# Optimization experiments

Hardware: AMD Instinct MI355X
Metric: run time of the kernel (lower is better)

The kernel has to match this reference:

```python
import jax, jax.numpy as jnp
import numpy as np

N = 20000
E = 640000
D = 128
NORM_FACTOR = 100.0
LN_EPS = 1e-5


def _layer_norm(x, g, b):
    mu = jnp.mean(x, axis=-1, keepdims=True)
    var = jnp.var(x, axis=-1, keepdims=True)
    return (x - mu) * jax.lax.rsqrt(var + LN_EPS) * g + b


def setup_inputs() -> dict:
    key = jax.random.key(0)
    ks = jax.random.split(key, 16)

    def lin(k, fan_in, shape):
        bound = 1.0 / np.sqrt(fan_in)
        return jax.random.uniform(k, shape, jnp.float32, -bound, bound)

    h = jax.random.normal(ks[0], (N, D), jnp.float32)
    distances = jax.random.uniform(ks[1], (E, 1), jnp.float32)
    edges = jax.random.randint(ks[2], (2, E), 0, N, jnp.int64)
    node_mask = jnp.ones((N, 1), jnp.float32)
    edge_mask = jnp.ones((E, 1), jnp.float32)

    return {
        "h": h, "distances": distances, "node_mask": node_mask, "edge_mask": edge_mask,
        # linear: in->out
        "lin_w": lin(ks[3], D, (D, D)), "lin_b": lin(ks[4], D, (D,)),
        # att_mlp: (2D+1)->2D -> 2D->D -> D->1
        "att_w1": lin(ks[5], 2 * D + 1, (2 * D, 2 * D + 1)), "att_b1": lin(ks[5], 2 * D + 1, (2 * D,)),
        "att_w2": lin(ks[6], 2 * D, (D, 2 * D)), "att_b2": lin(ks[6], 2 * D, (D,)),
        "att_w3": lin(ks[7], D, (1, D)), "att_b3": lin(ks[7], D, (1,)),
        # node_mlp: D->D, LN, SiLU, D->D
        "nm_w1": lin(ks[8], D, (D, D)), "nm_b1": lin(ks[8], D, (D,)),
        "nm_ln_g": jnp.ones((D,), jnp.float32), "nm_ln_b": jnp.zeros((D,), jnp.float32),
        "nm_w2": lin(ks[9], D, (D, D)), "nm_b2": lin(ks[9], D, (D,)),
        # final LayerNorm
        "ln_g": jnp.ones((D,), jnp.float32), "ln_b": jnp.zeros((D,), jnp.float32),
        "edges": edges,
    }


def reference(h, distances, node_mask, edge_mask,
              lin_w, lin_b, att_w1, att_b1, att_w2, att_b2, att_w3, att_b3,
              nm_w1, nm_b1, nm_ln_g, nm_ln_b, nm_w2, nm_b2, ln_g, ln_b, edges):
    x = h @ lin_w.T + lin_b                                  # [N, D]
    row, col = edges[0], edges[1]
    x_row = x[row]                                           # [E, D]
    x_col = x[col]                                           # [E, D]

    # DenseAtt
    d = distances * edge_mask
    x_cat = jnp.concatenate([x_row, x_col, d], axis=1)       # [E, 2D+1]
    a = jax.nn.silu(x_cat @ att_w1.T + att_b1)
    a = jax.nn.silu(a @ att_w2.T + att_b2)
    att = jax.nn.sigmoid(a @ att_w3.T + att_b3) * edge_mask  # [E, 1]

    agg = x_col * att                                        # [E, D]
    out = jax.ops.segment_sum(agg, row, num_segments=N) / NORM_FACTOR

    # node_mlp + residual
    o = out @ nm_w1.T + nm_b1
    o = jax.nn.silu(_layer_norm(o, nm_ln_g, nm_ln_b))
    o = o @ nm_w2.T + nm_b2
    hh = o + x

    hh = _layer_norm(hh, ln_g, ln_b)
    hh = jax.nn.silu(hh)                                     # act = SiLU
    return hh
```

## Files before the change

kernel.cpp:

```cpp
#include <hip/hip_runtime.h>
#include <hip/hip_bf16.h>

#define N_NODES 20000
#define E_EDGES 640000
#define DIM 128
#define CAP 96
#define EPB 64
#define NPB 8
#define XST 264

typedef __attribute__((ext_vector_type(8))) short bf16x8;
typedef __attribute__((ext_vector_type(4))) float f32x4;
typedef __attribute__((ext_vector_type(4))) unsigned u32x4;

#define LOG2E 1.44269504f
__device__ __forceinline__ float fsilu(float x) {
    return x * __builtin_amdgcn_rcpf(1.f + __builtin_amdgcn_exp2f(-LOG2E * x));
}
__device__ __forceinline__ float fsig(float x) {
    return __builtin_amdgcn_rcpf(1.f + __builtin_amdgcn_exp2f(-LOG2E * x));
}

__device__ __forceinline__ unsigned short f2bf(float x) {
    union { float f; unsigned u; } v; v.f = x;
    unsigned r = (v.u + 0x7fffu + ((v.u >> 16) & 1u)) >> 16;
    return (unsigned short)r;
}
__device__ __forceinline__ float bf2f(unsigned short s) {
    union { unsigned u; float f; } v; v.u = ((unsigned)s) << 16;
    return v.f;
}
__device__ __forceinline__ unsigned pack_bf16(float lo, float hi) {
    union { float f; unsigned u; } a, b; a.f = lo; b.f = hi;
    unsigned ul = a.u + 0x8000u, uh = b.u + 0x8000u;
    return __builtin_amdgcn_perm(uh, ul, 0x07060302u);
}

#define PRE_PREP_BLOCKS 64
#define PRE_LIN_BLOCKS  625
#define PRE_ADJ_BLOCKS  2500
__global__ __launch_bounds__(256) void pre_kernel(
    const float* __restrict__ w1, const float* __restrict__ w2,
    unsigned short* __restrict__ w1b, float* __restrict__ w1p,
    unsigned short* __restrict__ w2b,
    const float* __restrict__ h, const float* __restrict__ lw,
    const float* __restrict__ lb, float* __restrict__ x,
    unsigned short* __restrict__ xb,
    const int* __restrict__ edges,
    const float* __restrict__ dist, const float* __restrict__ emask,
    int* __restrict__ cnt,
    int* __restrict__ adjc, float2* __restrict__ dm, int E) {
    __shared__ float hs[32][128];
    int b = blockIdx.x;
    int t = threadIdx.x;

    if (b < PRE_PREP_BLOCKS) {
        int i = b * 256 + t;
        const int stride = PRE_PREP_BLOCKS * 256;
        for (int idx = i; idx < 256 * 256; idx += stride) {
            int o = idx >> 8, k = idx & 255;
            w1b[idx] = f2bf(w1[o * 257 + k]);
        }
        for (int idx = i; idx < 128 * 256; idx += stride) {
            int n2 = idx >> 8, p = idx & 255;
            int bb = p & ~31, off = p & 31;
            int ksrc = bb + (off >> 1) + ((off & 1) << 4);
            w2b[idx] = f2bf(w2[n2 * 256 + ksrc]);
        }
        for (int idx = i; idx < 256; idx += stride) {
            int bb = idx & ~31, off = idx & 31;
            int ksrc = bb + (off >> 1) + ((off & 1) << 4);
            w1p[idx] = w1[ksrc * 257 + 256];
        }
    } else if (b < PRE_PREP_BLOCKS + PRE_LIN_BLOCKS) {
        int nb = b - PRE_PREP_BLOCKS;
        int n0 = nb * 32;
        int ch = t & 127, g = t >> 7;
#pragma unroll
        for (int j = 0; j < 16; ++j) hs[g * 16 + j][ch] = h[(size_t)(n0 + g * 16 + j) * DIM + ch];
        __syncthreads();
        float acc[16];
#pragma unroll
        for (int j = 0; j < 16; ++j) acc[j] = 0.f;
        for (int kc = 0; kc < 128; kc += 4) {
            float4 wv = *(const float4*)&lw[(size_t)ch * DIM + kc];
#pragma unroll
            for (int j = 0; j < 16; ++j) {
                float4 hv = *(const float4*)&hs[g * 16 + j][kc];
                acc[j] += wv.x * hv.x + wv.y * hv.y + wv.z * hv.z + wv.w * hv.w;
            }
        }
        float bias = lb[ch];
#pragma unroll
        for (int j = 0; j < 16; ++j) {
            float v = acc[j] + bias;
            int n = n0 + g * 16 + j;
            x[(size_t)n * DIM + ch] = v;
            xb[(size_t)n * DIM + ch] = f2bf(v);
        }
    } else {
        int e = (b - PRE_PREP_BLOCKS - PRE_LIN_BLOCKS) * 256 + t;
        if (e < E) {
            int r = edges[e];
            int col = edges[E + e];
            float em = emask[e];
            float dv = dist[e] * em;
            int slot = atomicAdd(&cnt[r], 1);
            if (slot < CAP) {
                adjc[(size_t)r * CAP + slot] = col;
                float2 de; de.x = dv; de.y = em;
                dm[(size_t)r * CAP + slot] = de;
            }
        }
    }
}

__global__ __launch_bounds__(1024) void scan_kernel(const int* __restrict__ cnt,
                                                    int* __restrict__ off) {
    __shared__ int wsum[16], wbase[16];
    int t = threadIdx.x;
    int lane = t & 63, wid = t >> 6;
    int base = t * 20;
    int loc[20];
    int s = 0;
#pragma unroll
    for (int i = 0; i < 20; ++i) {
        int idx = base + i;
        int v = 0;
        if (idx < N_NODES) { v = cnt[idx]; v = v > CAP ? CAP : v; }
        loc[i] = s; s += v;
    }
    int inc = s;
#pragma unroll
    for (int d = 1; d < 64; d <<= 1) {
        int u = __shfl_up(inc, d);
        if (lane >= d) inc += u;
    }
    if (lane == 63) wsum[wid] = inc;
    __syncthreads();
    if (t < 16) {
        int v = wsum[t];
        int inc2 = v;
#pragma unroll
        for (int d = 1; d < 16; d <<= 1) {
            int u = __shfl_up(inc2, d);
            if (t >= d) inc2 += u;
        }
        wbase[t] = inc2 - v;
        if (t == 15) off[N_NODES] = inc2;
    }
    __syncthreads();
    int ex = wbase[wid] + inc - s;
#pragma unroll
    for (int i = 0; i < 20; ++i) {
        int idx = base + i;
        if (idx < N_NODES) off[idx] = ex + loc[i];
    }
}

#define MID_PRC_BLOCKS 1250
#define MID_FLAT_BLOCKS 2500
__global__ __launch_bounds__(256) void mid_kernel(
    const unsigned short* __restrict__ xb,
    const unsigned short* __restrict__ w1b,
    const float* __restrict__ b1,
    unsigned short* __restrict__ prb, unsigned short* __restrict__ pcb,
    const int* __restrict__ adjc, const float2* __restrict__ dm,
    const int* __restrict__ cnt, const int* __restrict__ off,
    int4* __restrict__ flat) {
    int b = blockIdx.x;
    if (b < MID_PRC_BLOCKS) {
        int n0 = b * 16;
        int w = threadIdx.x >> 6, lane = threadIdx.x & 63;
        int lrow = lane & 15, quad = lane >> 4;

        bf16x8 a[4];
#pragma unroll
        for (int kk = 0; kk < 4; ++kk)
            a[kk] = *(const bf16x8*)&xb[(size_t)(n0 + lrow) * DIM + kk * 32 + quad * 8];

        f32x4 z = {0.f, 0.f, 0.f, 0.f};
#pragma unroll
        for (int i = 0; i < 8; ++i) {
            int gt = w * 8 + i;
            int half = gt >> 4;
            int obase = (gt & 15) * 16;
            f32x4 acc = z;
#pragma unroll
            for (int kk = 0; kk < 4; ++kk) {
                bf16x8 bfrag = *(const bf16x8*)&w1b[(size_t)(obase + lrow) * 256 + half * 128 + kk * 32 + quad * 8];
                acc = __builtin_amdgcn_mfma_f32_16x16x32_bf16(a[kk], bfrag, acc, 0, 0, 0);
            }
            int o = obase + lrow;
            if (half == 0) {
                float bias = b1[o];
#pragma unroll
                for (int r = 0; r < 4; ++r)
                    prb[(size_t)(n0 + quad * 4 + r) * 256 + o] = f2bf(acc[r] + bias);
            } else {
#pragma unroll
                for (int r = 0; r < 4; ++r)
                    pcb[(size_t)(n0 + quad * 4 + r) * 256 + o] = f2bf(acc[r]);
            }
        }
    } else {
        int fb = b - MID_PRC_BLOCKS;
        int n0 = fb * NPB;
        int jg = threadIdx.x >> 5, l = threadIdx.x & 31;
        int n = n0 + jg;
        int c = cnt[n]; c = c > CAP ? CAP : c;
        int o = off[n];
        const int* al = adjc + (size_t)n * CAP;
        const float2* dl = dm + (size_t)n * CAP;
        for (int i = l; i < c; i += 32) {
            float2 de = dl[i];
            int4 wv;
            union { float f; int i; } u1, u2; u1.f = de.x; u2.f = de.y;
            wv.x = n; wv.y = al[i]; wv.z = u1.i; wv.w = u2.i;
            flat[o + i] = wv;
        }
    }
}

__global__ __launch_bounds__(512, 4) void edge_kernel(
    const unsigned short* __restrict__ prb, const unsigned short* __restrict__ pcb,
    const int4* __restrict__ flat, const int* __restrict__ off,
    const float* __restrict__ w1p,
    const unsigned short* __restrict__ w2b, const float* __restrict__ b2,
    const float* __restrict__ w3, const float* __restrict__ b3v,
    float* __restrict__ attv) {
    __shared__ unsigned short buf[EPB * XST];
    __shared__ float part[8][EPB];
    __shared__ float w1ps[256];

    int tid = threadIdx.x;
    int eb = blockIdx.x * EPB;
    int count = off[N_NODES];

    if (tid < 256) w1ps[tid] = w1p[tid];

    int ge = tid >> 3, cb = tid & 7;
    int eidx = eb + ge;
    int4 fv;
    if (eidx < count) fv = flat[eidx];
    else { fv.x = 0; fv.y = 0; fv.z = 0; fv.w = 0; }
    const unsigned short* prow = prb + (size_t)fv.x * 256 + cb * 32;
    const unsigned short* pcp  = pcb + (size_t)fv.y * 256 + cb * 32;
    union { int i; float f; } ud; ud.i = fv.z;
    float d = ud.f;

    bf16x8 pA0 = *(const bf16x8*)&prow[0];
    bf16x8 pB0 = *(const bf16x8*)&prow[16];
    bf16x8 qA0 = *(const bf16x8*)&pcp[0];
    bf16x8 qB0 = *(const bf16x8*)&pcp[16];
    bf16x8 pA1 = *(const bf16x8*)&prow[8];
    bf16x8 pB1 = *(const bf16x8*)&prow[24];
    bf16x8 qA1 = *(const bf16x8*)&pcp[8];
    bf16x8 qB1 = *(const bf16x8*)&pcp[24];

    int wave = tid >> 6, lane = tid & 63;
    int lrow = lane & 15, quad = lane >> 4;
    int n2 = wave * 16 + lrow;
    float bias2 = b2[n2];
    float w3v = w3[n2];

    __syncthreads();

    {
        const float* wp = &w1ps[cb * 32];
        unsigned u[16];
#pragma unroll
        for (int l = 0; l < 8; ++l) {
            float s0 = bf2f((unsigned short)pA0[l]) + bf2f((unsigned short)qA0[l]) + d * wp[2 * l];
            float s1 = bf2f((unsigned short)pB0[l]) + bf2f((unsigned short)qB0[l]) + d * wp[2 * l + 1];
            u[l] = pack_bf16(fsilu(s0), fsilu(s1));
        }
#pragma unroll
        for (int l = 0; l < 8; ++l) {
            float s0 = bf2f((unsigned short)pA1[l]) + bf2f((unsigned short)qA1[l]) + d * wp[16 + 2 * l];
            float s1 = bf2f((unsigned short)pB1[l]) + bf2f((unsigned short)qB1[l]) + d * wp[16 + 2 * l + 1];
            u[8 + l] = pack_bf16(fsilu(s0), fsilu(s1));
        }
        u32x4* w4 = (u32x4*)&buf[ge * XST + cb * 32];
        u32x4 v0 = {u[0], u[1], u[2], u[3]};
        u32x4 v1 = {u[4], u[5], u[6], u[7]};
        u32x4 v2 = {u[8], u[9], u[10], u[11]};
        u32x4 v3 = {u[12], u[13], u[14], u[15]};
        w4[0] = v0; w4[1] = v1; w4[2] = v2; w4[3] = v3;
    }
    __syncthreads();

    f32x4 zz = {0.f, 0.f, 0.f, 0.f};
    f32x4 acc2[4];
#pragma unroll
    for (int mt = 0; mt < 4; ++mt) acc2[mt] = zz;

    for (int kk = 0; kk < 8; ++kk) {
        int ka = kk * 32 + quad * 8;
        bf16x8 bfrag = *(const bf16x8*)&w2b[(size_t)n2 * 256 + ka];
#pragma unroll
        for (int mt = 0; mt < 4; ++mt) {
            bf16x8 a = *(bf16x8*)&buf[(mt * 16 + lrow) * XST + ka];
            acc2[mt] = __builtin_amdgcn_mfma_f32_16x16x32_bf16(a, bfrag, acc2[mt], 0, 0, 0);
        }
    }

    float s[4][4];
#pragma unroll
    for (int mt = 0; mt < 4; ++mt)
#pragma unroll
        for (int r = 0; r < 4; ++r)
            s[mt][r] = fsilu(acc2[mt][r] + bias2) * w3v;
#pragma unroll
    for (int off2 = 1; off2 < 16; off2 <<= 1) {
#pragma unroll
        for (int mt = 0; mt < 4; ++mt)
#pragma unroll
            for (int r = 0; r < 4; ++r)
                s[mt][r] += __shfl_xor(s[mt][r], off2);
    }
    if (lrow == 0) {
#pragma unroll
        for (int mt = 0; mt < 4; ++mt)
#pragma unroll
            for (int r = 0; r < 4; ++r)
                part[wave][mt * 16 + quad * 4 + r] = s[mt][r];
    }
    __syncthreads();

    if (tid < EPB) {
        int idx = eb + tid;
        if (idx < count) {
            float ssum = b3v[0];
#pragma unroll
            for (int w = 0; w < 8; ++w) ssum += part[w][tid];
            union { int i; float f; } ue; ue.i = flat[idx].w;
            attv[idx] = fsig(ssum) * ue.f;
        }
    }
}

__global__ __launch_bounds__(256) void node_kernel(
    const float* __restrict__ attv, const int* __restrict__ adjc,
    const int* __restrict__ cnt, const int* __restrict__ off,
    const unsigned short* __restrict__ xb,
    const float* __restrict__ x,
    const float* __restrict__ w1, const float* __restrict__ bb1,
    const float* __restrict__ lng, const float* __restrict__ lnb,
    const float* __restrict__ w2, const float* __restrict__ bb2,
    const float* __restrict__ gF, const float* __restrict__ bF,
    float* __restrict__ out, int E) {
    __shared__ float atts[NPB][CAP];
    __shared__ int   cols[NPB][CAP];
    __shared__ float outv[NPB][128];
    __shared__ float bufs[NPB][128];
    __shared__ float mu_s[NPB], rs_s[NPB];
    __shared__ int cnts[NPB];

    int t = threadIdx.x;
    int n0 = blockIdx.x * NPB;

    if (t < NPB) { int c = cnt[n0 + t]; cnts[t] = c > CAP ? CAP : c; }
    __syncthreads();

    {
        int jg = t >> 5, l = t & 31;
        int c = cnts[jg];
        const int* al = adjc + (size_t)(n0 + jg) * CAP;
        const float* av = attv + off[n0 + jg];
        for (int i = l; i < c; i += 32) {
            atts[jg][i] = av[i];
            cols[jg][i] = al[i];
        }
    }
    __syncthreads();

    int w = t >> 6, lane = t & 63;
    int islot = lane >> 4;
    int co = lane & 15;
#pragma unroll
    for (int jj = 0; jj < 2; ++jj) {
        int j = w * 2 + jj;
        int c = cnts[j];
        float acc[8];
#pragma unroll
        for (int k = 0; k < 8; ++k) acc[k] = 0.f;
        for (int base = 0; base < c; base += 8) {
            int i0 = base + islot, i1 = base + 4 + islot;
            bool k0 = i0 < c, k1 = i1 < c;
            int c0 = cols[j][k0 ? i0 : 0];
            int c1 = cols[j][k1 ? i1 : 0];
            float a0 = k0 ? atts[j][i0] : 0.f;
            float a1 = k1 ? atts[j][i1] : 0.f;
            bf16x8 q0 = *(const bf16x8*)&xb[(size_t)c0 * DIM + co * 8];
            bf16x8 q1 = *(const bf16x8*)&xb[(size_t)c1 * DIM + co * 8];
#pragma unroll
            for (int k = 0; k < 8; ++k) acc[k] += a0 * bf2f((unsigned short)q0[k]);
#pragma unroll
            for (int k = 0; k < 8; ++k) acc[k] += a1 * bf2f((unsigned short)q1[k]);
        }
#pragma unroll
        for (int k = 0; k < 8; ++k) {
            acc[k] += __shfl_xor(acc[k], 16);
            acc[k] += __shfl_xor(acc[k], 32);
        }
        if (islot == 0) {
            float4 v0 = {acc[0] * 0.01f, acc[1] * 0.01f, acc[2] * 0.01f, acc[3] * 0.01f};
            float4 v1 = {acc[4] * 0.01f, acc[5] * 0.01f, acc[6] * 0.01f, acc[7] * 0.01f};
            *(float4*)&outv[j][co * 8] = v0;
            *(float4*)&outv[j][co * 8 + 4] = v1;
        }
    }
    __syncthreads();

    int h = t >> 7, ch = t & 127;
    float xres[4];
#pragma unroll
    for (int jj = 0; jj < 4; ++jj)
        xres[jj] = x[(size_t)(n0 + h * 4 + jj) * DIM + ch];

    float a1[4] = {0, 0, 0, 0};
    for (int kc = 0; kc < 128; kc += 4) {
        float4 wv = *(const float4*)&w1[(size_t)ch * DIM + kc];
#pragma unroll
        for (int jj = 0; jj < 4; ++jj) {
            int j = h * 4 + jj;
            float4 ov = *(const float4*)&outv[j][kc];
            a1[jj] += wv.x * ov.x + wv.y * ov.y + wv.z * ov.z + wv.w * ov.w;
        }
    }
    float bias1 = bb1[ch];
#pragma unroll
    for (int jj = 0; jj < 4; ++jj) bufs[h * 4 + jj][ch] = a1[jj] + bias1;
    __syncthreads();

    {
        int j = t >> 5, l = t & 31;
        float s = 0.f, qq = 0.f;
#pragma unroll
        for (int i = 0; i < 4; ++i) { float v = bufs[j][l + 32 * i]; s += v; qq += v * v; }
#pragma unroll
        for (int off2 = 16; off2; off2 >>= 1) { s += __shfl_xor(s, off2); qq += __shfl_xor(qq, off2); }
        if (l == 0) {
            float mu = s * (1.f / 128.f);
            float var = qq * (1.f / 128.f) - mu * mu;
            mu_s[j] = mu; rs_s[j] = __builtin_amdgcn_rsqf(var + 1e-5f);
        }
    }
    __syncthreads();

    float g = lng[ch], bb = lnb[ch];
    float h2[4];
#pragma unroll
    for (int jj = 0; jj < 4; ++jj) {
        int j = h * 4 + jj;
        h2[jj] = fsilu((bufs[j][ch] - mu_s[j]) * rs_s[j] * g + bb);
    }
    __syncthreads();
#pragma unroll
    for (int jj = 0; jj < 4; ++jj) bufs[h * 4 + jj][ch] = h2[jj];
    __syncthreads();

    float a3[4] = {0, 0, 0, 0};
    for (int kc = 0; kc < 128; kc += 4) {
        float4 wv = *(const float4*)&w2[(size_t)ch * DIM + kc];
#pragma unroll
        for (int jj = 0; jj < 4; ++jj) {
            int j = h * 4 + jj;
            float4 bv = *(const float4*)&bufs[j][kc];
            a3[jj] += wv.x * bv.x + wv.y * bv.y + wv.z * bv.z + wv.w * bv.w;
        }
    }
    float bias2 = bb2[ch];
    float hh[4];
#pragma unroll
    for (int jj = 0; jj < 4; ++jj) hh[jj] = a3[jj] + bias2 + xres[jj];
    __syncthreads();
#pragma unroll
    for (int jj = 0; jj < 4; ++jj) bufs[h * 4 + jj][ch] = hh[jj];
    __syncthreads();

    {
        int j = t >> 5, l = t & 31;
        float s = 0.f, qq = 0.f;
#pragma unroll
        for (int i = 0; i < 4; ++i) { float v = bufs[j][l + 32 * i]; s += v; qq += v * v; }
#pragma unroll
        for (int off2 = 16; off2; off2 >>= 1) { s += __shfl_xor(s, off2); qq += __shfl_xor(qq, off2); }
        if (l == 0) {
            float mu = s * (1.f / 128.f);
            float var = qq * (1.f / 128.f) - mu * mu;
            mu_s[j] = mu; rs_s[j] = __builtin_amdgcn_rsqf(var + 1e-5f);
        }
    }
    __syncthreads();

    float gf = gF[ch], bf = bF[ch];
#pragma unroll
    for (int jj = 0; jj < 4; ++jj) {
        int j = h * 4 + jj;
        float y = (hh[jj] - mu_s[j]) * rs_s[j] * gf + bf;
        out[(size_t)(n0 + j) * DIM + ch] = fsilu(y);
    }
}

extern "C" void kernel_launch(void* const* d_in, const int* in_sizes, int n_in,
                              void* d_out, int out_size, void* d_ws, size_t ws_size,
                              hipStream_t stream) {
    const float* h         = (const float*)d_in[0];
    const float* distances = (const float*)d_in[1];
    const float* edge_mask = (const float*)d_in[3];
    const float* lin_w     = (const float*)d_in[4];
    const float* lin_b     = (const float*)d_in[5];
    const float* att_w1    = (const float*)d_in[6];
    const float* att_b1    = (const float*)d_in[7];
    const float* att_w2    = (const float*)d_in[8];
    const float* att_b2    = (const float*)d_in[9];
    const float* att_w3    = (const float*)d_in[10];
    const float* att_b3    = (const float*)d_in[11];
    const float* nm_w1     = (const float*)d_in[12];
    const float* nm_b1     = (const float*)d_in[13];
    const float* nm_ln_g   = (const float*)d_in[14];
    const float* nm_ln_b   = (const float*)d_in[15];
    const float* nm_w2     = (const float*)d_in[16];
    const float* nm_b2     = (const float*)d_in[17];
    const float* ln_g      = (const float*)d_in[18];
    const float* ln_b      = (const float*)d_in[19];
    const int*   edges     = (const int*)d_in[20];
    float* out = (float*)d_out;

    const int N = N_NODES, E = E_EDGES;

    char* ws = (char*)d_ws;
    float* x            = (float*)ws;            ws += (size_t)N * DIM * 4;
    unsigned short* xb  = (unsigned short*)ws;   ws += (size_t)N * DIM * 2;
    int* cnt            = (int*)ws;              ws += (size_t)N * 4;
    int* off            = (int*)ws;              ws += (size_t)(N + 4) * 4;
    int* adjc           = (int*)ws;              ws += (size_t)N * CAP * 4;
    float2* dm          = (float2*)ws;           ws += (size_t)N * CAP * 8;
    float* attv         = (float*)ws;            ws += (size_t)E * 4;
    unsigned short* w1b = (unsigned short*)ws;   ws += 256 * 256 * 2;
    float* w1p          = (float*)ws;            ws += 256 * 4;
    unsigned short* w2b = (unsigned short*)ws;   ws += 128 * 256 * 2;
    unsigned short* prb = (unsigned short*)ws;   ws += (size_t)N * 256 * 2;
    unsigned short* pcb = (unsigned short*)ws;   ws += (size_t)N * 256 * 2;
    int4* flat          = (int4*)ws;             ws += (size_t)E * 16;

    hipMemsetAsync(cnt, 0, (size_t)N * 4, stream);

    pre_kernel<<<PRE_PREP_BLOCKS + PRE_LIN_BLOCKS + PRE_ADJ_BLOCKS, 256, 0, stream>>>(
        att_w1, att_w2, w1b, w1p, w2b,
        h, lin_w, lin_b, x, xb,
        edges, distances, edge_mask, cnt, adjc, dm, E);
    scan_kernel<<<1, 1024, 0, stream>>>(cnt, off);
    mid_kernel<<<MID_PRC_BLOCKS + MID_FLAT_BLOCKS, 256, 0, stream>>>(
        xb, w1b, att_b1, prb, pcb, adjc, dm, cnt, off, flat);
    edge_kernel<<<E / EPB, 512, 0, stream>>>(prb, pcb, flat, off,
                                             w1p, w2b, att_b2,
                                             att_w3, att_b3, attv);
    node_kernel<<<N / NPB, 256, 0, stream>>>(attv, adjc, cnt, off, xb, x,
                                             nm_w1, nm_b1, nm_ln_g, nm_ln_b,
                                             nm_w2, nm_b2, ln_g, ln_b, out, E);
}
```

Baseline: 417.9 us.

## Scatter edges directly into CSR flat array and drop padded adjacency buffers

Edge bucketing becomes two passes. The first pass only counts degrees with atomics. A second scatter pass in mid_kernel writes each edge straight into the scanned CSR flat array, using a second counter. This removes the padded per-node adjc/dm buffers and the copy that compacted them. The edge kernel now stores attention in the flat array's fourth field instead of a separate attv buffer, and node_kernel reads cols and att from flat. The SiLU in the edge kernel's first layer is also rewritten on float2 vectors so packed math can be used. The trade-off is reading the edge arrays twice and adding a second round of atomics, and edge order within a node is now nondeterministic.

```diff
diff --git a/kernel.cpp b/kernel.cpp
--- a/kernel.cpp
+++ b/kernel.cpp
@@ -11,6 +11,7 @@
 
 typedef __attribute__((ext_vector_type(8))) short bf16x8;
 typedef __attribute__((ext_vector_type(4))) float f32x4;
+typedef __attribute__((ext_vector_type(2))) float f32x2;
 typedef __attribute__((ext_vector_type(4))) unsigned u32x4;
 
 #define LOG2E 1.44269504f
@@ -19,6 +20,13 @@
 }
 __device__ __forceinline__ float fsig(float x) {
     return __builtin_amdgcn_rcpf(1.f + __builtin_amdgcn_exp2f(-LOG2E * x));
+}
+__device__ __forceinline__ f32x2 fsilu2(f32x2 v) {
+    f32x2 m = v * (-LOG2E);
+    f32x2 e; e.x = __builtin_amdgcn_exp2f(m.x); e.y = __builtin_amdgcn_exp2f(m.y);
+    f32x2 den = e + 1.0f;
+    f32x2 r; r.x = __builtin_amdgcn_rcpf(den.x); r.y = __builtin_amdgcn_rcpf(den.y);
+    return v * r;
 }
 
 __device__ __forceinline__ unsigned short f2bf(float x) {
@@ -38,7 +46,7 @@
 
 #define PRE_PREP_BLOCKS 64
 #define PRE_LIN_BLOCKS  625
-#define PRE_ADJ_BLOCKS  2500
+#define PRE_CNT_BLOCKS  2500
 __global__ __launch_bounds__(256) void pre_kernel(
     const float* __restrict__ w1, const float* __restrict__ w2,
     unsigned short* __restrict__ w1b, float* __restrict__ w1p,
@@ -46,10 +54,7 @@
     const float* __restrict__ h, const float* __restrict__ lw,
     const float* __restrict__ lb, float* __restrict__ x,
     unsigned short* __restrict__ xb,
-    const int* __restrict__ edges,
-    const float* __restrict__ dist, const float* __restrict__ emask,
-    int* __restrict__ cnt,
-    int* __restrict__ adjc, float2* __restrict__ dm, int E) {
+    const int* __restrict__ edges, int* __restrict__ cnt, int E) {
     __shared__ float hs[32][128];
     int b = blockIdx.x;
     int t = threadIdx.x;
@@ -100,18 +105,7 @@
         }
     } else {
         int e = (b - PRE_PREP_BLOCKS - PRE_LIN_BLOCKS) * 256 + t;
-        if (e < E) {
-            int r = edges[e];
-            int col = edges[E + e];
-            float em = emask[e];
-            float dv = dist[e] * em;
-            int slot = atomicAdd(&cnt[r], 1);
-            if (slot < CAP) {
-                adjc[(size_t)r * CAP + slot] = col;
-                float2 de; de.x = dv; de.y = em;
-                dm[(size_t)r * CAP + slot] = de;
-            }
-        }
+        if (e < E) atomicAdd(&cnt[edges[e]], 1);
     }
 }
 
@@ -159,15 +153,16 @@
 }
 
 #define MID_PRC_BLOCKS 1250
-#define MID_FLAT_BLOCKS 2500
+#define MID_SCAT_BLOCKS 2500
 __global__ __launch_bounds__(256) void mid_kernel(
     const unsigned short* __restrict__ xb,
     const unsigned short* __restrict__ w1b,
     const float* __restrict__ b1,
     unsigned short* __restrict__ prb, unsigned short* __restrict__ pcb,
-    const int* __restrict__ adjc, const float2* __restrict__ dm,
-    const int* __restrict__ cnt, const int* __restrict__ off,
-    int4* __restrict__ flat) {
+    const int* __restrict__ edges,
+    const float* __restrict__ dist, const float* __restrict__ emask,
+    int* __restrict__ cnt2, const int* __restrict__ off,
+    int4* __restrict__ flat, int E) {
     int b = blockIdx.x;
     if (b < MID_PRC_BLOCKS) {
         int n0 = b * 16;
@@ -204,31 +199,29 @@
             }
         }
     } else {
-        int fb = b - MID_PRC_BLOCKS;
-        int n0 = fb * NPB;
-        int jg = threadIdx.x >> 5, l = threadIdx.x & 31;
-        int n = n0 + jg;
-        int c = cnt[n]; c = c > CAP ? CAP : c;
-        int o = off[n];
-        const int* al = adjc + (size_t)n * CAP;
-        const float2* dl = dm + (size_t)n * CAP;
-        for (int i = l; i < c; i += 32) {
-            float2 de = dl[i];
-            int4 wv;
-            union { float f; int i; } u1, u2; u1.f = de.x; u2.f = de.y;
-            wv.x = n; wv.y = al[i]; wv.z = u1.i; wv.w = u2.i;
-            flat[o + i] = wv;
+        int e = (b - MID_PRC_BLOCKS) * 256 + threadIdx.x;
+        if (e < E) {
+            int r = edges[e];
+            int col = edges[E + e];
+            float em = emask[e];
+            float dv = dist[e] * em;
+            int slot = atomicAdd(&cnt2[r], 1);
+            if (slot < CAP) {
+                int4 wv;
+                union { float f; int i; } u1, u2; u1.f = dv; u2.f = em;
+                wv.x = r; wv.y = col; wv.z = u1.i; wv.w = u2.i;
+                flat[off[r] + slot] = wv;
+            }
         }
     }
 }
 
 __global__ __launch_bounds__(512, 4) void edge_kernel(
     const unsigned short* __restrict__ prb, const unsigned short* __restrict__ pcb,
-    const int4* __restrict__ flat, const int* __restrict__ off,
+    int4* __restrict__ flat, const int* __restrict__ off,
     const float* __restrict__ w1p,
     const unsigned short* __restrict__ w2b, const float* __restrict__ b2,
-    const float* __restrict__ w3, const float* __restrict__ b3v,
-    float* __restrict__ attv) {
+    const float* __restrict__ w3, const float* __restrict__ b3v) {
     __shared__ unsigned short buf[EPB * XST];
     __shared__ float part[8][EPB];
     __shared__ float w1ps[256];
@@ -268,18 +261,23 @@
 
     {
         const float* wp = &w1ps[cb * 32];
+        f32x2 d2 = {d, d};
         unsigned u[16];
 #pragma unroll
         for (int l = 0; l < 8; ++l) {
-            float s0 = bf2f((unsigned short)pA0[l]) + bf2f((unsigned short)qA0[l]) + d * wp[2 * l];
-            float s1 = bf2f((unsigned short)pB0[l]) + bf2f((unsigned short)qB0[l]) + d * wp[2 * l + 1];
-            u[l] = pack_bf16(fsilu(s0), fsilu(s1));
+            f32x2 p = {bf2f((unsigned short)pA0[l]), bf2f((unsigned short)pB0[l])};
+            f32x2 q = {bf2f((unsigned short)qA0[l]), bf2f((unsigned short)qB0[l])};
+            f32x2 wv2 = *(const f32x2*)&wp[2 * l];
+            f32x2 sv = fsilu2(p + q + d2 * wv2);
+            u[l] = pack_bf16(sv.x, sv.y);
         }
 #pragma unroll
         for (int l = 0; l < 8; ++l) {
-            float s0 = bf2f((unsigned short)pA1[l]) + bf2f((unsigned short)qA1[l]) + d * wp[16 + 2 * l];
-            float s1 = bf2f((unsigned short)pB1[l]) + bf2f((unsigned short)qB1[l]) + d * wp[16 + 2 * l + 1];
-            u[8 + l] = pack_bf16(fsilu(s0), fsilu(s1));
+            f32x2 p = {bf2f((unsigned short)pA1[l]), bf2f((unsigned short)pB1[l])};
+            f32x2 q = {bf2f((unsigned short)qA1[l]), bf2f((unsigned short)qB1[l])};
+            f32x2 wv2 = *(const f32x2*)&wp[16 + 2 * l];
+            f32x2 sv = fsilu2(p + q + d2 * wv2);
+            u[8 + l] = pack_bf16(sv.x, sv.y);
         }
         u32x4* w4 = (u32x4*)&buf[ge * XST + cb * 32];
         u32x4 v0 = {u[0], u[1], u[2], u[3]};
@@ -335,13 +333,14 @@
 #pragma unroll
             for (int w = 0; w < 8; ++w) ssum += part[w][tid];
             union { int i; float f; } ue; ue.i = flat[idx].w;
-            attv[idx] = fsig(ssum) * ue.f;
+            union { float f; int i; } ua; ua.f = fsig(ssum) * ue.f;
+            ((int*)&flat[idx])[3] = ua.i;
         }
     }
 }
 
 __global__ __launch_bounds__(256) void node_kernel(
-    const float* __restrict__ attv, const int* __restrict__ adjc,
+    const int4* __restrict__ flat,
     const int* __restrict__ cnt, const int* __restrict__ off,
     const unsigned short* __restrict__ xb,
     const float* __restrict__ x,
@@ -366,11 +365,12 @@
     {
         int jg = t >> 5, l = t & 31;
         int c = cnts[jg];
-        const int* al = adjc + (size_t)(n0 + jg) * CAP;
-        const float* av = attv + off[n0 + jg];
+        const int4* fl = flat + off[n0 + jg];
         for (int i = l; i < c; i += 32) {
-            atts[jg][i] = av[i];
-            cols[jg][i] = al[i];
+            int4 v = fl[i];
+            union { int i; float f; } ua; ua.i = v.w;
+            atts[jg][i] = ua.f;
+            cols[jg][i] = v.y;
         }
     }
     __syncthreads();
@@ -535,30 +535,27 @@
     float* x            = (float*)ws;            ws += (size_t)N * DIM * 4;
     unsigned short* xb  = (unsigned short*)ws;   ws += (size_t)N * DIM * 2;
     int* cnt            = (int*)ws;              ws += (size_t)N * 4;
+    int* cnt2           = (int*)ws;              ws += (size_t)N * 4;
     int* off            = (int*)ws;              ws += (size_t)(N + 4) * 4;
-    int* adjc           = (int*)ws;              ws += (size_t)N * CAP * 4;
-    float2* dm          = (float2*)ws;           ws += (size_t)N * CAP * 8;
-    float* attv         = (float*)ws;            ws += (size_t)E * 4;
+    int4* flat          = (int4*)ws;             ws += (size_t)E * 16;
     unsigned short* w1b = (unsigned short*)ws;   ws += 256 * 256 * 2;
     float* w1p          = (float*)ws;            ws += 256 * 4;
     unsigned short* w2b = (unsigned short*)ws;   ws += 128 * 256 * 2;
     unsigned short* prb = (unsigned short*)ws;   ws += (size_t)N * 256 * 2;
     unsigned short* pcb = (unsigned short*)ws;   ws += (size_t)N * 256 * 2;
-    int4* flat          = (int4*)ws;             ws += (size_t)E * 16;
-
-    hipMemsetAsync(cnt, 0, (size_t)N * 4, stream);
-
-    pre_kernel<<<PRE_PREP_BLOCKS + PRE_LIN_BLOCKS + PRE_ADJ_BLOCKS, 256, 0, stream>>>(
+
+    hipMemsetAsync(cnt, 0, (size_t)N * 8, stream);
+
+    pre_kernel<<<PRE_PREP_BLOCKS + PRE_LIN_BLOCKS + PRE_CNT_BLOCKS, 256, 0, stream>>>(
         att_w1, att_w2, w1b, w1p, w2b,
         h, lin_w, lin_b, x, xb,
-        edges, distances, edge_mask, cnt, adjc, dm, E);
+        edges, cnt, E);
     scan_kernel<<<1, 1024, 0, stream>>>(cnt, off);
-    mid_kernel<<<MID_PRC_BLOCKS + MID_FLAT_BLOCKS, 256, 0, stream>>>(
-        xb, w1b, att_b1, prb, pcb, adjc, dm, cnt, off, flat);
+    mid_kernel<<<MID_PRC_BLOCKS + MID_SCAT_BLOCKS, 256, 0, stream>>>(
+        xb, w1b, att_b1, prb, pcb, edges, distances, edge_mask, cnt2, off, flat, E);
     edge_kernel<<<E / EPB, 512, 0, stream>>>(prb, pcb, flat, off,
-                                             w1p, w2b, att_b2,
-                                             att_w3, att_b3, attv);
-    node_kernel<<<N / NPB, 256, 0, stream>>>(attv, adjc, cnt, off, xb, x,
+                                             w1p, w2b, att_b2, att_w3, att_b3);
+    node_kernel<<<N / NPB, 256, 0, stream>>>(flat, cnt, off, xb, x,
                                              nm_w1, nm_b1, nm_ln_g, nm_ln_b,
                                              nm_w2, nm_b2, ln_g, ln_b, out, E);
 }
```

New measurement: 441.2 us. 1.06x slower.
